# Performance work log

Hardware: AMD Instinct MI355X
Metric: run time of the kernel (lower is better)

Reference implementation:

```python
import jax, jax.numpy as jnp
import numpy as np

B, CIN, CMID, H, W, K, PAD = 2, 192, 180, 96, 96, 3, 1


def conv1x1(x, w, b):
    # x: [B,C,H,W], w: [O,C], b: [O]
    return jnp.einsum('bchw,oc->bohw', x, w) + b[None, :, None, None]


def deform_conv2d(x, offset, weight, bias, pad=PAD):
    """torchvision-style DeformConv2d, stride=1, dilation=1, mask=None.
    x: [B,C,H,W]; offset: [B, 2*G*K*K, H, W] with (y,x) pairs per kernel tap;
    weight: [Cout, C, K, K]; bias: [Cout]."""
    Bx, C, Hx, Wx = x.shape
    Cout, Cin, Kk, _ = weight.shape
    KK = Kk * Kk
    G = offset.shape[1] // (2 * KK)          # offset groups (10 here)
    Cg = C // G
    off = offset.reshape(Bx, G, KK, 2, Hx, Wx)
    hh = jnp.arange(Hx, dtype=x.dtype)
    ww = jnp.arange(Wx, dtype=x.dtype)
    kys = (jnp.arange(KK) // Kk).astype(x.dtype) - pad
    kxs = (jnp.arange(KK) % Kk).astype(x.dtype) - pad
    # sampling coords: [B,G,KK,H,W]
    sy = off[:, :, :, 0] + kys[None, None, :, None, None] + hh[None, None, None, :, None]
    sx = off[:, :, :, 1] + kxs[None, None, :, None, None] + ww[None, None, None, None, :]
    y0f = jnp.floor(sy); x0f = jnp.floor(sx)
    dy = sy - y0f; dx = sx - x0f
    y0 = y0f.astype(jnp.int32); x0 = x0f.astype(jnp.int32)
    xg = x.reshape(Bx, G, Cg, Hx * Wx)

    def gather(yi, xi, wgt):
        valid = (yi >= 0) & (yi < Hx) & (xi >= 0) & (xi < Wx)
        idx = jnp.clip(yi, 0, Hx - 1) * Wx + jnp.clip(xi, 0, Wx - 1)
        idx = idx.reshape(Bx, G, 1, KK * Hx * Wx)
        v = jnp.take_along_axis(xg, idx, axis=3)          # [B,G,Cg,KK*H*W]
        wv = (wgt * valid.astype(x.dtype)).reshape(Bx, G, 1, KK * Hx * Wx)
        return v * wv

    val = (gather(y0, x0, (1 - dy) * (1 - dx))
           + gather(y0, x0 + 1, (1 - dy) * dx)
           + gather(y0 + 1, x0, dy * (1 - dx))
           + gather(y0 + 1, x0 + 1, dy * dx))
    patches = val.reshape(Bx, C, KK, Hx, Wx)              # [B,Cin,KK,H,W]
    out = jnp.einsum('bikhw,oik->bohw', patches, weight.reshape(Cout, Cin, KK))
    return out + bias[None, :, None, None]


def setup_inputs() -> dict:
    key = jax.random.key(0)
    ks = jax.random.split(key, 14)
    s = 0.05
    return {
        'x': jax.random.normal(ks[0], (B, CIN, H, W), jnp.float32),
        'w_reduce': jax.random.normal(ks[1], (CMID, CIN), jnp.float32) * s,
        'b_reduce': jax.random.normal(ks[2], (CMID,), jnp.float32) * s,
        'w_offset': jax.random.normal(ks[3], (2 * CMID, CMID), jnp.float32) * s,
        'b_offset': jax.random.normal(ks[4], (2 * CMID,), jnp.float32) * s,
        'w_dcnw': jax.random.normal(ks[5], (CMID, CMID, K, K), jnp.float32) * s,
        'b_dcnw': jax.random.normal(ks[6], (CMID,), jnp.float32) * s,
        'w_dcnh': jax.random.normal(ks[7], (CMID, CMID, K, K), jnp.float32) * s,
        'b_dcnh': jax.random.normal(ks[8], (CMID,), jnp.float32) * s,
        'w_expand': jax.random.normal(ks[9], (CIN, CMID), jnp.float32) * s,
        'b_expand': jax.random.normal(ks[10], (CIN,), jnp.float32) * s,
        'w_attn': jax.random.normal(ks[11], (2, CMID), jnp.float32) * s,
        'b_attn': jax.random.normal(ks[12], (2,), jnp.float32) * s,
    }


def reference(x, w_reduce, b_reduce, w_offset, b_offset, w_dcnw, b_dcnw,
              w_dcnh, b_dcnh, w_expand, b_expand, w_attn, b_attn):
    xr = conv1x1(x, w_reduce, b_reduce)                     # [B,CMID,H,W]
    offs = conv1x1(xr, w_offset, b_offset)                  # [B,2*CMID,H,W]
    cm = xr.shape[1]
    off_w, off_h = offs[:, :cm], offs[:, cm:]
    f_w = deform_conv2d(xr, off_w, w_dcnw, b_dcnw)
    f_h = deform_conv2d(xr, off_h, w_dcnh, b_dcnh)
    f_avg = (f_w + f_h).mean(axis=(2, 3), keepdims=True)    # [B,CMID,1,1]
    attn = jax.nn.softmax(conv1x1(f_avg, w_attn, b_attn), axis=1)  # [B,2,1,1]
    f_dcm = attn[:, 0:1] * f_h + attn[:, 1:2] * f_w
    return conv1x1(f_dcm, w_expand, b_expand)
```

## Files before the change

### kernel.cpp

```cpp
#include <hip/hip_runtime.h>
#include <math.h>

#define HH 96
#define WW 96
#define HW 9216
#define CIN 192
#define CMID 180
#define NB 2
#define NG 10
#define KTAPS 9
#define KP 1760
#define GCH 176
#define NDW 880
#define MP 192
#define CP 20

typedef __attribute__((ext_vector_type(8))) short short8;
typedef __attribute__((ext_vector_type(4))) float f32x4;
union FragU { uint2 u2[2]; short8 v; };

static __device__ inline unsigned short f2bf(float f) {
    unsigned x = __float_as_uint(f);
    unsigned r = (x + 0x7fffu + ((x >> 16) & 1u)) >> 16;
    return (unsigned short)r;
}
#define SWZ(r) ((((r) & 3) << 4) | (((r) & 4) << 1))

template<bool COMBINE, bool XT>
__global__ __launch_bounds__(256)
void gemm_k(const float* __restrict__ A,
            const float* __restrict__ B0, const float* __restrict__ B1,
            const float* __restrict__ attnb,
            const float* __restrict__ bias, float* __restrict__ C,
            float* __restrict__ xrt,
            int M, int N, int K, int ldb, int ldc, int bsB, int bsC)
{
    const int b = blockIdx.z;
    const float* Bp0 = B0 + (size_t)b * bsB;
    const float* Bp1 = COMBINE ? (B1 + (size_t)b * bsB) : nullptr;
    float* Cp = C + (size_t)b * bsC;
    float a0 = 0.f, a1 = 0.f;
    if (COMBINE) { a0 = attnb[2*b]; a1 = attnb[2*b+1]; }

    __shared__ float As[16][68];
    __shared__ float Bs[16][64];

    const int tid = threadIdx.x;
    const int m0 = blockIdx.x * 64, n0 = blockIdx.y * 64;
    const int am = tid >> 2, ak = (tid & 3) << 2;
    const int bk = tid >> 4, bn = (tid & 15) << 2;
    const int ty = tid >> 4, tx = tid & 15;

    float acc[4][4] = {};

    for (int k0 = 0; k0 < K; k0 += 16) {
        float4 av = make_float4(0.f, 0.f, 0.f, 0.f);
        if ((m0 + am) < M && (k0 + ak) < K)
            av = *reinterpret_cast<const float4*>(A + (size_t)(m0 + am) * K + k0 + ak);
        As[ak + 0][am] = av.x; As[ak + 1][am] = av.y;
        As[ak + 2][am] = av.z; As[ak + 3][am] = av.w;

        float4 bv = make_float4(0.f, 0.f, 0.f, 0.f);
        if ((k0 + bk) < K) {
            size_t o = (size_t)(k0 + bk) * ldb + n0 + bn;
            bv = *reinterpret_cast<const float4*>(Bp0 + o);
            if (COMBINE) {
                float4 c4 = *reinterpret_cast<const float4*>(Bp1 + o);
                bv.x = a0 * bv.x + a1 * c4.x; bv.y = a0 * bv.y + a1 * c4.y;
                bv.z = a0 * bv.z + a1 * c4.z; bv.w = a0 * bv.w + a1 * c4.w;
            }
        }
        *reinterpret_cast<float4*>(&Bs[bk][bn]) = bv;
        __syncthreads();

        #pragma unroll
        for (int kk = 0; kk < 16; ++kk) {
            float4 a  = *reinterpret_cast<const float4*>(&As[kk][ty << 2]);
            float4 bb = *reinterpret_cast<const float4*>(&Bs[kk][tx << 2]);
            acc[0][0] += a.x * bb.x; acc[0][1] += a.x * bb.y; acc[0][2] += a.x * bb.z; acc[0][3] += a.x * bb.w;
            acc[1][0] += a.y * bb.x; acc[1][1] += a.y * bb.y; acc[1][2] += a.y * bb.z; acc[1][3] += a.y * bb.w;
            acc[2][0] += a.z * bb.x; acc[2][1] += a.z * bb.y; acc[2][2] += a.z * bb.z; acc[2][3] += a.z * bb.w;
            acc[3][0] += a.w * bb.x; acc[3][1] += a.w * bb.y; acc[3][2] += a.w * bb.z; acc[3][3] += a.w * bb.w;
        }
        __syncthreads();
    }

    #pragma unroll
    for (int i = 0; i < 4; ++i) {
        int m = m0 + (ty << 2) + i;
        if (m < M) {
            float bi = bias[m];
            #pragma unroll
            for (int j = 0; j < 4; ++j) {
                float s = acc[i][j] + bi;
                int n = n0 + (tx << 2) + j;
                Cp[(size_t)m * ldc + n] = s;
                if (XT)
                    xrt[((size_t)(b * NG + m / 18) * HW + n) * CP + (m % 18)] = s;
            }
        }
    }
}

__global__ __launch_bounds__(256)
void convw5_k(const float* __restrict__ w0, const float* __restrict__ w1,
              unsigned short* __restrict__ wbf)
{
    int idx = blockIdx.x * 256 + threadIdx.x;
    int set = idx / (MP * KP);
    int r0 = idx - set * MP * KP;
    int o = r0 / KP, k = r0 - o * KP;
    int g = k / GCH, kr = k - g * GCH;
    float v = 0.f;
    if (o < CMID && kr < 162) {
        int kk = kr / 18, c = kr % 18;
        v = (set ? w1 : w0)[((size_t)o * CMID + g * 18 + c) * KTAPS + kk];
    }
    wbf[idx] = f2bf(v);
}

__global__ __launch_bounds__(256)
void gather6_k(const float* __restrict__ xrt, const float* __restrict__ offs,
               unsigned* __restrict__ patch2, int set, int p0, int nchunk)
{
    const int b = blockIdx.z;
    const int g = blockIdx.y;
    const int pl = blockIdx.x * 256 + threadIdx.x;
    const int pix = p0 + pl;
    const int h = pix / WW, w = pix % WW;

    const float* ob = offs + (((size_t)b * 2 + set) * CMID + g * 18) * HW + pix;
    float oyA[9], oxA[9];
    #pragma unroll
    for (int kk = 0; kk < 9; ++kk) {
        oyA[kk] = ob[(size_t)(2 * kk) * HW];
        oxA[kk] = ob[(size_t)(2 * kk + 1) * HW];
    }

    const float* gbase = xrt + (size_t)(b * NG + g) * HW * CP;
    unsigned u[88];
    #pragma unroll
    for (int i = 81; i < 88; ++i) u[i] = 0u;

    #pragma unroll
    for (int kk = 0; kk < 9; ++kk) {
        float sy = oyA[kk] + (float)(kk / 3 - 1 + h);
        float sx = oxA[kk] + (float)(kk % 3 - 1 + w);
        float yf = floorf(sy), xf = floorf(sx);
        float dy = sy - yf, dx = sx - xf;
        int y0 = (int)yf, x0 = (int)xf;
        bool vy0 = (unsigned)y0 < (unsigned)HH, vy1 = (unsigned)(y0 + 1) < (unsigned)HH;
        bool vx0 = (unsigned)x0 < (unsigned)WW, vx1 = (unsigned)(x0 + 1) < (unsigned)WW;
        int yc0 = min(max(y0, 0), HH - 1), yc1 = min(max(y0 + 1, 0), HH - 1);
        int xc0 = min(max(x0, 0), WW - 1), xc1 = min(max(x0 + 1, 0), WW - 1);
        float w00 = (1.f - dy) * (1.f - dx) * ((vy0 && vx0) ? 1.f : 0.f);
        float w01 = (1.f - dy) * dx         * ((vy0 && vx1) ? 1.f : 0.f);
        float w10 = dy * (1.f - dx)         * ((vy1 && vx0) ? 1.f : 0.f);
        float w11 = dy * dx                 * ((vy1 && vx1) ? 1.f : 0.f);

        const float* r00 = gbase + (size_t)(yc0 * WW + xc0) * CP;
        const float* r01 = gbase + (size_t)(yc0 * WW + xc1) * CP;
        const float* r10 = gbase + (size_t)(yc1 * WW + xc0) * CP;
        const float* r11 = gbase + (size_t)(yc1 * WW + xc1) * CP;

        float A00[18], A01[18], A10[18], A11[18];
        #pragma unroll
        for (int q = 0; q < 4; ++q) {
            *reinterpret_cast<float4*>(&A00[q * 4]) = *reinterpret_cast<const float4*>(r00 + q * 4);
            *reinterpret_cast<float4*>(&A01[q * 4]) = *reinterpret_cast<const float4*>(r01 + q * 4);
            *reinterpret_cast<float4*>(&A10[q * 4]) = *reinterpret_cast<const float4*>(r10 + q * 4);
            *reinterpret_cast<float4*>(&A11[q * 4]) = *reinterpret_cast<const float4*>(r11 + q * 4);
        }
        *reinterpret_cast<float2*>(&A00[16]) = *reinterpret_cast<const float2*>(r00 + 16);
        *reinterpret_cast<float2*>(&A01[16]) = *reinterpret_cast<const float2*>(r01 + 16);
        *reinterpret_cast<float2*>(&A10[16]) = *reinterpret_cast<const float2*>(r10 + 16);
        *reinterpret_cast<float2*>(&A11[16]) = *reinterpret_cast<const float2*>(r11 + 16);

        #pragma unroll
        for (int c = 0; c < 18; c += 2) {
            float v0 = w00 * A00[c]     + w01 * A01[c]     + w10 * A10[c]     + w11 * A11[c];
            float v1 = w00 * A00[c + 1] + w01 * A01[c + 1] + w10 * A10[c + 1] + w11 * A11[c + 1];
            u[kk * 9 + (c >> 1)] = (unsigned)f2bf(v0) | ((unsigned)f2bf(v1) << 16);
        }
    }

    unsigned* dst = patch2 + ((size_t)(b * NDW) + g * 88) * nchunk + pl;
    #pragma unroll
    for (int i = 0; i < 88; ++i)
        dst[(size_t)i * nchunk] = u[i];
}

__global__ __launch_bounds__(256)
void dgemm_k(const unsigned short* __restrict__ A, const unsigned* __restrict__ patch2,
             const float* __restrict__ bias, float* __restrict__ C, int nchunk, int p0)
{
    __shared__ uint4 smem[1024];
    char* lds = (char*)smem;
    const int b = blockIdx.z, n0 = blockIdx.x * 64;
    const int tid = threadIdx.x;
    const int wv = tid >> 6, l = tid & 63;
    const int lg = l >> 4, lm = l & 15;
    const int arow = tid >> 2, aseg = tid & 3;
    const int bdw = tid & 15, bpq = tid >> 4;

    const unsigned short* Ag = A + (size_t)arow * KP + aseg * 8;
    const unsigned* Bg = patch2 + (size_t)(b * NDW) * nchunk + n0 + 4 * bpq;

    int wbA[3], wmA[3];
    #pragma unroll
    for (int i = 0; i < 3; ++i) {
        int row = arow + (i << 6);
        wbA[i] = row << 6;
        wmA[i] = (aseg << 4) ^ SWZ(row);
    }
    int wB[4];
    #pragma unroll
    for (int i = 0; i < 4; ++i) {
        int n = bpq * 4 + i;
        wB[i] = 12288 + (n << 6) + ((bdw << 2) ^ SWZ(n));
    }

    int aoff[3][2], boff[4][2];
    #pragma unroll
    for (int fr = 0; fr < 3; ++fr) {
        int row = wv * 48 + fr * 16 + lm;
        int m = SWZ(row);
        aoff[fr][0] = (row << 6) + (((lg << 3)     ) ^ m);
        aoff[fr][1] = (row << 6) + (((lg << 3) + 32) ^ m);
    }
    #pragma unroll
    for (int nc = 0; nc < 4; ++nc) {
        int n = nc * 16 + lm;
        int m = SWZ(n);
        boff[nc][0] = 12288 + (n << 6) + (((lg << 3)     ) ^ m);
        boff[nc][1] = 12288 + (n << 6) + (((lg << 3) + 32) ^ m);
    }

    uint4 ra0 = *(const uint4*)(Ag);
    uint4 ra1 = *(const uint4*)(Ag + (size_t)64 * KP);
    uint4 ra2 = *(const uint4*)(Ag + (size_t)128 * KP);
    uint4 rb  = *(const uint4*)(Bg + (size_t)bdw * nchunk);

    f32x4 acc[3][4];
    #pragma unroll
    for (int i = 0; i < 3; ++i)
        #pragma unroll
        for (int j = 0; j < 4; ++j)
            acc[i][j] = (f32x4){0.f, 0.f, 0.f, 0.f};

    for (int kt = 0; kt < KP / 32; ++kt) {
        __syncthreads();
        *(uint2*)(lds + wbA[0] + wmA[0])       = make_uint2(ra0.x, ra0.y);
        *(uint2*)(lds + wbA[0] + (wmA[0] ^ 8)) = make_uint2(ra0.z, ra0.w);
        *(uint2*)(lds + wbA[1] + wmA[1])       = make_uint2(ra1.x, ra1.y);
        *(uint2*)(lds + wbA[1] + (wmA[1] ^ 8)) = make_uint2(ra1.z, ra1.w);
        *(uint2*)(lds + wbA[2] + wmA[2])       = make_uint2(ra2.x, ra2.y);
        *(uint2*)(lds + wbA[2] + (wmA[2] ^ 8)) = make_uint2(ra2.z, ra2.w);
        *(unsigned*)(lds + wB[0]) = rb.x;
        *(unsigned*)(lds + wB[1]) = rb.y;
        *(unsigned*)(lds + wB[2]) = rb.z;
        *(unsigned*)(lds + wB[3]) = rb.w;
        __syncthreads();

        if (kt < KP / 32 - 1) {
            int k0 = (kt + 1) * 32;
            ra0 = *(const uint4*)(Ag + k0);
            ra1 = *(const uint4*)(Ag + (size_t)64 * KP + k0);
            ra2 = *(const uint4*)(Ag + (size_t)128 * KP + k0);
            rb  = *(const uint4*)(Bg + (size_t)((kt + 1) * 16 + bdw) * nchunk);
        }

        FragU af[3], bf[4];
        #pragma unroll
        for (int fr = 0; fr < 3; ++fr) {
            af[fr].u2[0] = *(const uint2*)(lds + aoff[fr][0]);
            af[fr].u2[1] = *(const uint2*)(lds + aoff[fr][1]);
        }
        #pragma unroll
        for (int nc = 0; nc < 4; ++nc) {
            bf[nc].u2[0] = *(const uint2*)(lds + boff[nc][0]);
            bf[nc].u2[1] = *(const uint2*)(lds + boff[nc][1]);
        }
        #pragma unroll
        for (int fr = 0; fr < 3; ++fr)
            #pragma unroll
            for (int nc = 0; nc < 4; ++nc)
                acc[fr][nc] = __builtin_amdgcn_mfma_f32_16x16x32_bf16(
                    af[fr].v, bf[nc].v, acc[fr][nc], 0, 0, 0);
    }

    #pragma unroll
    for (int fr = 0; fr < 3; ++fr) {
        #pragma unroll
        for (int r = 0; r < 4; ++r) {
            int rr = wv * 48 + fr * 16 + lg * 4 + r;
            if (rr < CMID) {
                float bi = bias[rr];
                float* Cr = C + (size_t)b * CMID * HW + (size_t)rr * HW + p0 + n0 + lm;
                #pragma unroll
                for (int nc = 0; nc < 4; ++nc)
                    Cr[nc * 16] = acc[fr][nc][r] + bi;
            }
        }
    }
}

__global__ __launch_bounds__(256)
void avg_k(const float* __restrict__ fw, const float* __restrict__ fh,
           float* __restrict__ favg)
{
    const int bm = blockIdx.x;
    const size_t base = (size_t)bm * HW;
    float s = 0.f;
    for (int i = threadIdx.x; i < HW; i += 256)
        s += fw[base + i] + fh[base + i];
    #pragma unroll
    for (int off = 32; off > 0; off >>= 1) s += __shfl_down(s, off, 64);
    __shared__ float sb[4];
    const int tid = threadIdx.x;
    if ((tid & 63) == 0) sb[tid >> 6] = s;
    __syncthreads();
    if (tid == 0) favg[bm] = (sb[0] + sb[1] + sb[2] + sb[3]) / (float)HW;
}

__global__ __launch_bounds__(256)
void attn_k(const float* __restrict__ favg, const float* __restrict__ w_attn,
            const float* __restrict__ b_attn, float* __restrict__ attnb)
{
    const int b = blockIdx.x;
    const int t = threadIdx.x;
    float z0 = 0.f, z1 = 0.f;
    if (t < CMID) {
        float f = favg[b * CMID + t];
        z0 = w_attn[t] * f;
        z1 = w_attn[CMID + t] * f;
    }
    #pragma unroll
    for (int off = 32; off > 0; off >>= 1) {
        z0 += __shfl_down(z0, off, 64);
        z1 += __shfl_down(z1, off, 64);
    }
    __shared__ float s0[4], s1[4];
    if ((t & 63) == 0) { s0[t >> 6] = z0; s1[t >> 6] = z1; }
    __syncthreads();
    if (t == 0) {
        float a = s0[0] + s0[1] + s0[2] + s0[3] + b_attn[0];
        float c = s1[0] + s1[1] + s1[2] + s1[3] + b_attn[1];
        float m = fmaxf(a, c);
        float e0 = expf(a - m), e1 = expf(c - m);
        float inv = 1.f / (e0 + e1);
        attnb[2 * b + 0] = e0 * inv;
        attnb[2 * b + 1] = e1 * inv;
    }
}

extern "C" void kernel_launch(void* const* d_in, const int* in_sizes, int n_in,
                              void* d_out, int out_size, void* d_ws, size_t ws_size,
                              hipStream_t stream) {
    const float* x        = (const float*)d_in[0];
    const float* w_reduce = (const float*)d_in[1];
    const float* b_reduce = (const float*)d_in[2];
    const float* w_offset = (const float*)d_in[3];
    const float* b_offset = (const float*)d_in[4];
    const float* w_dcnw   = (const float*)d_in[5];
    const float* b_dcnw   = (const float*)d_in[6];
    const float* w_dcnh   = (const float*)d_in[7];
    const float* b_dcnh   = (const float*)d_in[8];
    const float* w_expand = (const float*)d_in[9];
    const float* b_expand = (const float*)d_in[10];
    const float* w_attn   = (const float*)d_in[11];
    const float* b_attn   = (const float*)d_in[12];
    float* out = (float*)d_out;

    char* base = (char*)d_ws;
    size_t o = 0;
    float* xr    = (float*)(base + o); o += (size_t)NB * CMID * HW * 4;
    float* offs  = (float*)(base + o); o += (size_t)NB * 2 * CMID * HW * 4;
    float* fw    = (float*)(base + o); o += (size_t)NB * CMID * HW * 4;
    float* fh    = (float*)(base + o); o += (size_t)NB * CMID * HW * 4;
    float* favg  = (float*)(base + o); o += (size_t)NB * CMID * 4;
    float* attnb = (float*)(base + o); o += 32;
    float* xrt   = (float*)(base + o); o += (size_t)NB * NG * HW * CP * 4;
    unsigned short* wbf = (unsigned short*)(base + o); o += (size_t)2 * MP * KP * 2;
    unsigned* patch2 = (unsigned*)(base + o);

    int nchunk = 2304;
    const int cand[3] = {9216, 4608, 2304};
    for (int i = 0; i < 3; ++i) {
        size_t need = o + (size_t)NB * cand[i] * KP * 2;
        if (need <= ws_size) { nchunk = cand[i]; break; }
    }

    convw5_k<<<dim3((2 * MP * KP) / 256), 256, 0, stream>>>(w_dcnw, w_dcnh, wbf);

    gemm_k<false, true><<<dim3(3, HW / 64, NB), 256, 0, stream>>>(
        w_reduce, x, nullptr, nullptr, b_reduce, xr, xrt,
        CMID, HW, CIN, HW, HW, CIN * HW, CMID * HW);

    gemm_k<false, false><<<dim3(6, HW / 64, NB), 256, 0, stream>>>(
        w_offset, xr, nullptr, nullptr, b_offset, offs, nullptr,
        2 * CMID, HW, CMID, HW, HW, CMID * HW, 2 * CMID * HW);

    for (int set = 0; set < 2; ++set) {
        const float* bD = set ? b_dcnh : b_dcnw;
        float* fD = set ? fh : fw;
        for (int p0 = 0; p0 < HW; p0 += nchunk) {
            gather6_k<<<dim3(nchunk / 256, NG, NB), 256, 0, stream>>>(
                xrt, offs, patch2, set, p0, nchunk);
            dgemm_k<<<dim3(nchunk / 64, 1, NB), 256, 0, stream>>>(
                wbf + (size_t)set * MP * KP, patch2, bD, fD, nchunk, p0);
        }
    }

    avg_k<<<dim3(NB * CMID), 256, 0, stream>>>(fw, fh, favg);

    attn_k<<<dim3(NB), 256, 0, stream>>>(favg, w_attn, b_attn, attnb);

    gemm_k<true, false><<<dim3(3, HW / 64, NB), 256, 0, stream>>>(
        w_expand, fh, fw, attnb, b_expand, out, nullptr,
        CIN, HW, CMID, HW, HW, CMID * HW, CIN * HW);
}
```

Before: 409.9 us.

## Batch both deformable conv sets per launch and double-buffer LDS in dgemm

Merges the two deformable-conv sets into single gather and GEMM launches by folding the set index into the grid. This doubles parallelism per launch and halves the launch count. The dgemm kernel gains double-buffered shared memory, so the next K-tile is stored while the current one feeds the MFMAs, and one barrier per iteration is dropped. The patch buffer doubles in size, which may force a smaller chunk size if workspace is limited, and the doubled LDS may lower occupancy.

```diff
diff --git a/kernel.cpp b/kernel.cpp
--- a/kernel.cpp
+++ b/kernel.cpp
@@ -121,15 +121,16 @@
 
 __global__ __launch_bounds__(256)
 void gather6_k(const float* __restrict__ xrt, const float* __restrict__ offs,
-               unsigned* __restrict__ patch2, int set, int p0, int nchunk)
-{
-    const int b = blockIdx.z;
+               unsigned* __restrict__ patch2, int p0, int nchunk)
+{
+    const int z = blockIdx.z;
+    const int b = z >> 1;
     const int g = blockIdx.y;
     const int pl = blockIdx.x * 256 + threadIdx.x;
     const int pix = p0 + pl;
     const int h = pix / WW, w = pix % WW;
 
-    const float* ob = offs + (((size_t)b * 2 + set) * CMID + g * 18) * HW + pix;
+    const float* ob = offs + ((size_t)z * CMID + g * 18) * HW + pix;
     float oyA[9], oxA[9];
     #pragma unroll
     for (int kk = 0; kk < 9; ++kk) {
@@ -184,27 +185,28 @@
         }
     }
 
-    unsigned* dst = patch2 + ((size_t)(b * NDW) + g * 88) * nchunk + pl;
+    unsigned* dst = patch2 + ((size_t)z * NDW + g * 88) * nchunk + pl;
     #pragma unroll
     for (int i = 0; i < 88; ++i)
         dst[(size_t)i * nchunk] = u[i];
 }
 
 __global__ __launch_bounds__(256)
-void dgemm_k(const unsigned short* __restrict__ A, const unsigned* __restrict__ patch2,
-             const float* __restrict__ bias, float* __restrict__ C, int nchunk, int p0)
-{
-    __shared__ uint4 smem[1024];
+void dgemm_k(const unsigned short* __restrict__ wbfA, const unsigned* __restrict__ patch2,
+             const float* __restrict__ bW, const float* __restrict__ bH,
+             float* __restrict__ fw, float* __restrict__ fh, int nchunk, int p0)
+{
+    __shared__ uint4 smem[2048];
     char* lds = (char*)smem;
-    const int b = blockIdx.z, n0 = blockIdx.x * 64;
+    const int set = blockIdx.y, b = blockIdx.z, n0 = blockIdx.x * 64;
     const int tid = threadIdx.x;
     const int wv = tid >> 6, l = tid & 63;
     const int lg = l >> 4, lm = l & 15;
     const int arow = tid >> 2, aseg = tid & 3;
     const int bdw = tid & 15, bpq = tid >> 4;
 
-    const unsigned short* Ag = A + (size_t)arow * KP + aseg * 8;
-    const unsigned* Bg = patch2 + (size_t)(b * NDW) * nchunk + n0 + 4 * bpq;
+    const unsigned short* Ag = wbfA + (size_t)set * MP * KP + (size_t)arow * KP + aseg * 8;
+    const unsigned* Bg = patch2 + (size_t)((b * 2 + set) * NDW) * nchunk + n0 + 4 * bpq;
 
     int wbA[3], wmA[3];
     #pragma unroll
@@ -236,50 +238,72 @@
         boff[nc][1] = 12288 + (n << 6) + (((lg << 3) + 32) ^ m);
     }
 
+    f32x4 acc[3][4];
+    #pragma unroll
+    for (int i = 0; i < 3; ++i)
+        #pragma unroll
+        for (int j = 0; j < 4; ++j)
+            acc[i][j] = (f32x4){0.f, 0.f, 0.f, 0.f};
+
+    const int NT = KP / 32;
+
     uint4 ra0 = *(const uint4*)(Ag);
     uint4 ra1 = *(const uint4*)(Ag + (size_t)64 * KP);
     uint4 ra2 = *(const uint4*)(Ag + (size_t)128 * KP);
     uint4 rb  = *(const uint4*)(Bg + (size_t)bdw * nchunk);
-
-    f32x4 acc[3][4];
-    #pragma unroll
-    for (int i = 0; i < 3; ++i)
-        #pragma unroll
-        for (int j = 0; j < 4; ++j)
-            acc[i][j] = (f32x4){0.f, 0.f, 0.f, 0.f};
-
-    for (int kt = 0; kt < KP / 32; ++kt) {
-        __syncthreads();
-        *(uint2*)(lds + wbA[0] + wmA[0])       = make_uint2(ra0.x, ra0.y);
-        *(uint2*)(lds + wbA[0] + (wmA[0] ^ 8)) = make_uint2(ra0.z, ra0.w);
-        *(uint2*)(lds + wbA[1] + wmA[1])       = make_uint2(ra1.x, ra1.y);
-        *(uint2*)(lds + wbA[1] + (wmA[1] ^ 8)) = make_uint2(ra1.z, ra1.w);
-        *(uint2*)(lds + wbA[2] + wmA[2])       = make_uint2(ra2.x, ra2.y);
-        *(uint2*)(lds + wbA[2] + (wmA[2] ^ 8)) = make_uint2(ra2.z, ra2.w);
-        *(unsigned*)(lds + wB[0]) = rb.x;
-        *(unsigned*)(lds + wB[1]) = rb.y;
-        *(unsigned*)(lds + wB[2]) = rb.z;
-        *(unsigned*)(lds + wB[3]) = rb.w;
-        __syncthreads();
-
-        if (kt < KP / 32 - 1) {
-            int k0 = (kt + 1) * 32;
-            ra0 = *(const uint4*)(Ag + k0);
-            ra1 = *(const uint4*)(Ag + (size_t)64 * KP + k0);
-            ra2 = *(const uint4*)(Ag + (size_t)128 * KP + k0);
-            rb  = *(const uint4*)(Bg + (size_t)((kt + 1) * 16 + bdw) * nchunk);
-        }
-
+    {
+        char* L = lds;
+        *(uint2*)(L + wbA[0] + wmA[0])       = make_uint2(ra0.x, ra0.y);
+        *(uint2*)(L + wbA[0] + (wmA[0] ^ 8)) = make_uint2(ra0.z, ra0.w);
+        *(uint2*)(L + wbA[1] + wmA[1])       = make_uint2(ra1.x, ra1.y);
+        *(uint2*)(L + wbA[1] + (wmA[1] ^ 8)) = make_uint2(ra1.z, ra1.w);
+        *(uint2*)(L + wbA[2] + wmA[2])       = make_uint2(ra2.x, ra2.y);
+        *(uint2*)(L + wbA[2] + (wmA[2] ^ 8)) = make_uint2(ra2.z, ra2.w);
+        *(unsigned*)(L + wB[0]) = rb.x;
+        *(unsigned*)(L + wB[1]) = rb.y;
+        *(unsigned*)(L + wB[2]) = rb.z;
+        *(unsigned*)(L + wB[3]) = rb.w;
+    }
+    ra0 = *(const uint4*)(Ag + 32);
+    ra1 = *(const uint4*)(Ag + (size_t)64 * KP + 32);
+    ra2 = *(const uint4*)(Ag + (size_t)128 * KP + 32);
+    rb  = *(const uint4*)(Bg + (size_t)(16 + bdw) * nchunk);
+    __syncthreads();
+
+    int cb = 0;
+    for (int kt = 0; kt < NT; ++kt) {
+        const int nb = cb ^ 16384;
+        if (kt + 1 < NT) {
+            char* L = lds + nb;
+            *(uint2*)(L + wbA[0] + wmA[0])       = make_uint2(ra0.x, ra0.y);
+            *(uint2*)(L + wbA[0] + (wmA[0] ^ 8)) = make_uint2(ra0.z, ra0.w);
+            *(uint2*)(L + wbA[1] + wmA[1])       = make_uint2(ra1.x, ra1.y);
+            *(uint2*)(L + wbA[1] + (wmA[1] ^ 8)) = make_uint2(ra1.z, ra1.w);
+            *(uint2*)(L + wbA[2] + wmA[2])       = make_uint2(ra2.x, ra2.y);
+            *(uint2*)(L + wbA[2] + (wmA[2] ^ 8)) = make_uint2(ra2.z, ra2.w);
+            *(unsigned*)(L + wB[0]) = rb.x;
+            *(unsigned*)(L + wB[1]) = rb.y;
+            *(unsigned*)(L + wB[2]) = rb.z;
+            *(unsigned*)(L + wB[3]) = rb.w;
+            if (kt + 2 < NT) {
+                const int k0 = (kt + 2) * 32;
+                ra0 = *(const uint4*)(Ag + k0);
+                ra1 = *(const uint4*)(Ag + (size_t)64 * KP + k0);
+                ra2 = *(const uint4*)(Ag + (size_t)128 * KP + k0);
+                rb  = *(const uint4*)(Bg + (size_t)((kt + 2) * 16 + bdw) * nchunk);
+            }
+        }
+        char* Lc = lds + cb;
         FragU af[3], bf[4];
         #pragma unroll
         for (int fr = 0; fr < 3; ++fr) {
-            af[fr].u2[0] = *(const uint2*)(lds + aoff[fr][0]);
-            af[fr].u2[1] = *(const uint2*)(lds + aoff[fr][1]);
+            af[fr].u2[0] = *(const uint2*)(Lc + aoff[fr][0]);
+            af[fr].u2[1] = *(const uint2*)(Lc + aoff[fr][1]);
         }
         #pragma unroll
         for (int nc = 0; nc < 4; ++nc) {
-            bf[nc].u2[0] = *(const uint2*)(lds + boff[nc][0]);
-            bf[nc].u2[1] = *(const uint2*)(lds + boff[nc][1]);
+            bf[nc].u2[0] = *(const uint2*)(Lc + boff[nc][0]);
+            bf[nc].u2[1] = *(const uint2*)(Lc + boff[nc][1]);
         }
         #pragma unroll
         for (int fr = 0; fr < 3; ++fr)
@@ -287,8 +311,12 @@
             for (int nc = 0; nc < 4; ++nc)
                 acc[fr][nc] = __builtin_amdgcn_mfma_f32_16x16x32_bf16(
                     af[fr].v, bf[nc].v, acc[fr][nc], 0, 0, 0);
-    }
-
+        __syncthreads();
+        cb = nb;
+    }
+
+    const float* bias = set ? bH : bW;
+    float* fD = set ? fh : fw;
     #pragma unroll
     for (int fr = 0; fr < 3; ++fr) {
         #pragma unroll
@@ -296,7 +324,7 @@
             int rr = wv * 48 + fr * 16 + lg * 4 + r;
             if (rr < CMID) {
                 float bi = bias[rr];
-                float* Cr = C + (size_t)b * CMID * HW + (size_t)rr * HW + p0 + n0 + lm;
+                float* Cr = fD + (size_t)b * CMID * HW + (size_t)rr * HW + p0 + n0 + lm;
                 #pragma unroll
                 for (int nc = 0; nc < 4; ++nc)
                     Cr[nc * 16] = acc[fr][nc][r] + bi;
@@ -387,7 +415,7 @@
     int nchunk = 2304;
     const int cand[3] = {9216, 4608, 2304};
     for (int i = 0; i < 3; ++i) {
-        size_t need = o + (size_t)NB * cand[i] * KP * 2;
+        size_t need = o + (size_t)NB * 2 * cand[i] * KP * 2;
         if (need <= ws_size) { nchunk = cand[i]; break; }
     }
 
@@ -401,15 +429,11 @@
         w_offset, xr, nullptr, nullptr, b_offset, offs, nullptr,
         2 * CMID, HW, CMID, HW, HW, CMID * HW, 2 * CMID * HW);
 
-    for (int set = 0; set < 2; ++set) {
-        const float* bD = set ? b_dcnh : b_dcnw;
-        float* fD = set ? fh : fw;
-        for (int p0 = 0; p0 < HW; p0 += nchunk) {
-            gather6_k<<<dim3(nchunk / 256, NG, NB), 256, 0, stream>>>(
-                xrt, offs, patch2, set, p0, nchunk);
-            dgemm_k<<<dim3(nchunk / 64, 1, NB), 256, 0, stream>>>(
-                wbf + (size_t)set * MP * KP, patch2, bD, fD, nchunk, p0);
-        }
+    for (int p0 = 0; p0 < HW; p0 += nchunk) {
+        gather6_k<<<dim3(nchunk / 256, NG, NB * 2), 256, 0, stream>>>(
+            xrt, offs, patch2, p0, nchunk);
+        dgemm_k<<<dim3(nchunk / 64, 2, NB), 256, 0, stream>>>(
+            wbf, patch2, b_dcnw, b_dcnh, fw, fh, nchunk, p0);
     }
 
     avg_k<<<dim3(NB * CMID), 256, 0, stream>>>(fw, fh, favg);
```

New measurement: 364.8 us. 11.0% less time.
